# Kernel optimization log

Measured on AMD Instinct MI355X. Metric: run time of the kernel, lower is better.

Reference implementation:

```python
import jax, jax.numpy as jnp
from jax import lax
import numpy as np

EPS_LN = 1e-5
EPS_BN = 1e-5
NEG_SLOPE = 0.01  # MONAI UnetResBlock leaky relu slope


def conv3d(x, w, b=None, padding=0, dilation=1, groups=1):
    # x: [B,C,D1,D2,D3], w: [O, I/groups, k,k,k]
    pads = [(padding, padding)] * 3
    y = lax.conv_general_dilated(x, w, (1, 1, 1), pads,
                                 rhs_dilation=(dilation,) * 3,
                                 dimension_numbers=('NCDHW', 'OIDHW', 'NCDHW'),
                                 feature_group_count=groups)
    if b is not None:
        y = y + b[None, :, None, None, None]
    return y


def _trilinear(x_flat, z, y, xw, D, H, W):
    # x_flat: [B,C,S]; z,y,xw: [B,S] float sample coords. Zero padding outside.
    z0 = jnp.floor(z); y0 = jnp.floor(y); x0 = jnp.floor(xw)
    tz = z - z0; ty = y - y0; tx = xw - x0
    iz0 = z0.astype(jnp.int32); iy0 = y0.astype(jnp.int32); ix0 = x0.astype(jnp.int32)
    gather = jax.vmap(lambda xf, i: jnp.take(xf, i, axis=1))  # over batch
    out = jnp.zeros_like(x_flat)
    for dz in (0, 1):
        for dy in (0, 1):
            for dx in (0, 1):
                zi = iz0 + dz; yi = iy0 + dy; xi = ix0 + dx
                wgt = ((tz if dz else 1.0 - tz) * (ty if dy else 1.0 - ty)
                       * (tx if dx else 1.0 - tx))
                valid = ((zi >= 0) & (zi < D) & (yi >= 0) & (yi < H)
                         & (xi >= 0) & (xi < W))
                idx = (jnp.clip(zi, 0, D - 1) * H + jnp.clip(yi, 0, H - 1)) * W \
                      + jnp.clip(xi, 0, W - 1)
                g = gather(x_flat, idx)  # [B,C,S]
                out = out + g * (wgt * valid)[:, None, :]
    return out


def deform_conv3d(x, off_w, off_b, w, b):
    # DCNv1-style 3D deformable conv, kernel 3x3x3, stride 1, pad 1.
    B, C, D, H, W = x.shape
    S = D * H * W
    off = conv3d(x, off_w, off_b, padding=1)          # [B, 3*27, D,H,W]
    off = off.reshape(B, 27, 3, S)                    # per-tap (dz,dy,dx)
    gz, gy, gx = jnp.meshgrid(jnp.arange(D), jnp.arange(H), jnp.arange(W), indexing='ij')
    gz = gz.reshape(-1).astype(x.dtype)
    gy = gy.reshape(-1).astype(x.dtype)
    gx = gx.reshape(-1).astype(x.dtype)
    x_flat = x.reshape(B, C, S)
    out = jnp.zeros((B, w.shape[0], S), x.dtype)
    k = 0
    for kd in (-1, 0, 1):
        for kh in (-1, 0, 1):
            for kw in (-1, 0, 1):
                z = gz[None, :] + kd + off[:, k, 0]
                y = gy[None, :] + kh + off[:, k, 1]
                xc = gx[None, :] + kw + off[:, k, 2]
                val = _trilinear(x_flat, z, y, xc, D, H, W)  # [B,C,S]
                out = out + jnp.einsum('oc,bcs->bos', w[:, :, kd + 1, kh + 1, kw + 1], val)
                k += 1
    out = out + b[None, :, None]
    return out.reshape(B, w.shape[0], D, H, W)


def _leaky(v):
    return jnp.where(v >= 0, v, NEG_SLOPE * v)


def _bn(v, s, b_, m, var):
    inv = lax.rsqrt(var + EPS_BN)
    return (v - m[None, :, None, None, None]) * (s * inv)[None, :, None, None, None] \
        + b_[None, :, None, None, None]


def reference(x, ln_s, ln_b, gamma,
              p1_w, p1_b, p2_w, p2_b,
              c0_w, c0_b, cs_w, cs_b,
              off_w, off_b, dc_w, dc_b,
              c1_w, c1_b,
              u1_w, bn1_s, bn1_b, bn1_m, bn1_v,
              u2_w, bn2_s, bn2_b, bn2_m, bn2_v,
              pr_w, pr_b):
    B, C, H, W, D = x.shape
    tok = x.reshape(B, C, -1).transpose(0, 2, 1)  # [B, N, C]
    # LayerNorm over C
    mu = jnp.mean(tok, axis=-1, keepdims=True)
    var = jnp.mean((tok - mu) ** 2, axis=-1, keepdims=True)
    xn = (tok - mu) * lax.rsqrt(var + EPS_LN) * ln_s + ln_b
    # _Attention3d_deform
    v = xn.transpose(0, 2, 1).reshape(B, C, H, W, D)
    shortcut = v
    v = conv3d(v, p1_w, p1_b)                 # proj_1 (1x1x1)
    v = jax.nn.gelu(v, approximate=False)
    # _3d_deform spatial gating unit
    u = v
    a = conv3d(v, c0_w, c0_b, padding=2, groups=C)              # 5x5x5 depthwise
    a = conv3d(a, cs_w, cs_b, padding=9, dilation=3, groups=C)  # 7x7x7 dil=3 depthwise
    a = deform_conv3d(a, off_w, off_b, dc_w, dc_b)
    a = conv3d(a, c1_w, c1_b)                 # 1x1x1
    v = u * a
    v = conv3d(v, p2_w, p2_b) + shortcut      # proj_2 + residual
    epa = v.reshape(B, C, -1).transpose(0, 2, 1)
    feat = tok + gamma * epa                  # [B, N, C]
    skip = feat.reshape(B, H, W, D, C).transpose(0, 4, 1, 2, 3)  # [B,C,H,W,D]
    # UnetResBlock (conv-bn-lrelu-conv-bn + residual, lrelu), eval-mode BN
    h = conv3d(skip, u1_w, padding=1)
    h = _leaky(_bn(h, bn1_s, bn1_b, bn1_m, bn1_v))
    h = conv3d(h, u2_w, padding=1)
    h = _bn(h, bn2_s, bn2_b, bn2_m, bn2_v)
    attn = _leaky(h + skip)
    # projconv: Dropout3d is identity in eval; 1x1x1 conv
    out = skip + conv3d(attn, pr_w, pr_b)
    return out


def setup_inputs() -> dict:
    key = jax.random.key(0)
    ks = jax.random.split(key, 16)
    C, Bv, S = 48, 2, 32

    def w(k, shape, s=0.05):
        return jax.random.normal(k, shape, jnp.float32) * s

    return {
        'x': jax.random.normal(ks[0], (Bv, C, S, S, S), jnp.float32),
        'ln_s': jnp.ones((C,), jnp.float32), 'ln_b': jnp.zeros((C,), jnp.float32),
        'gamma': jnp.full((C,), 0.1, jnp.float32),
        'p1_w': w(ks[1], (C, C, 1, 1, 1)), 'p1_b': jnp.zeros((C,), jnp.float32),
        'p2_w': w(ks[2], (C, C, 1, 1, 1)), 'p2_b': jnp.zeros((C,), jnp.float32),
        'c0_w': w(ks[3], (C, 1, 5, 5, 5)), 'c0_b': jnp.zeros((C,), jnp.float32),
        'cs_w': w(ks[4], (C, 1, 7, 7, 7)), 'cs_b': jnp.zeros((C,), jnp.float32),
        'off_w': w(ks[5], (81, C, 3, 3, 3), 0.01), 'off_b': jnp.zeros((81,), jnp.float32),
        'dc_w': w(ks[6], (C, C, 3, 3, 3)), 'dc_b': jnp.zeros((C,), jnp.float32),
        'c1_w': w(ks[7], (C, C, 1, 1, 1)), 'c1_b': jnp.zeros((C,), jnp.float32),
        'u1_w': w(ks[8], (C, C, 3, 3, 3)),
        'bn1_s': jnp.ones((C,), jnp.float32), 'bn1_b': jnp.zeros((C,), jnp.float32),
        'bn1_m': jnp.zeros((C,), jnp.float32), 'bn1_v': jnp.ones((C,), jnp.float32),
        'u2_w': w(ks[9], (C, C, 3, 3, 3)),
        'bn2_s': jnp.ones((C,), jnp.float32), 'bn2_b': jnp.zeros((C,), jnp.float32),
        'bn2_m': jnp.zeros((C,), jnp.float32), 'bn2_v': jnp.ones((C,), jnp.float32),
        'pr_w': w(ks[10], (C, C, 1, 1, 1)), 'pr_b': jnp.zeros((C,), jnp.float32),
    }
```

## Files before the change

kernel.cpp:

```cpp
#include <hip/hip_runtime.h>
#include <hip/hip_fp16.h>
#include <math.h>

#define CCH 48
#define SDIM 32
#define SVOL (SDIM*SDIM*SDIM)
#define NB 2

typedef _Float16 half2_t __attribute__((ext_vector_type(2)));
typedef _Float16 half4_t __attribute__((ext_vector_type(4)));
typedef float float4_t __attribute__((ext_vector_type(4)));

static __device__ __forceinline__ float dot2f(half2_t a, half2_t b, float c) {
#if __has_builtin(__builtin_amdgcn_fdot2)
    return __builtin_amdgcn_fdot2(a, b, c, false);
#else
    return c + (float)a[0] * (float)b[0] + (float)a[1] * (float)b[1];
#endif
}


__global__ __launch_bounds__(256)
void reshape_pair_kernel(const float* __restrict__ w, half2_t* __restrict__ wt, int NO) {
    int i = blockIdx.x * 256 + threadIdx.x;
    int total = 27 * 24 * NO;
    if (i < total) {
        int o = i % NO; int rem = i / NO; int cp = rem % 24; int k = rem / 24;
        float w0 = w[((size_t)o * CCH + 2 * cp) * 27 + k];
        float w1 = w[((size_t)o * CCH + 2 * cp + 1) * 27 + k];
        wt[i] = half2_t{ (_Float16)w0, (_Float16)w1 };
    }
}

__global__ __launch_bounds__(256)
void reshape_mfma_off_kernel(const float* __restrict__ w, half4_t* __restrict__ wA) {
    int e = blockIdx.x * 256 + threadIdx.x;
    if (e < 31104) {
        int row = e & 15;
        int kq = (e >> 4) & 3;
        int ks = (e / 64) % 3;
        int mt = (e / 192) % 6;
        int tap = e / 1152;
        int o = mt * 16 + row;
        half4_t v;
        #pragma unroll
        for (int h = 0; h < 4; h++) {
            int ci = ks * 16 + kq * 4 + h;
            float val = (o < 81) ? w[((size_t)o * CCH + ci) * 27 + tap] : 0.f;
            v[h] = (_Float16)val;
        }
        wA[e] = v;
    }
}

__global__ __launch_bounds__(256)
void reshape_mfma48_kernel(const float* __restrict__ w, half4_t* __restrict__ wA) {
    int e = blockIdx.x * 256 + threadIdx.x;
    if (e < 15552) {
        int row = e & 15;
        int kq = (e >> 4) & 3;
        int ks = (e / 64) % 3;
        int mt = (e / 192) % 3;
        int tap = e / 576;
        int o = mt * 16 + row;
        half4_t v;
        #pragma unroll
        for (int h = 0; h < 4; h++) {
            int ci = ks * 16 + kq * 4 + h;
            v[h] = (_Float16)w[((size_t)o * CCH + ci) * 27 + tap];
        }
        wA[e] = v;
    }
}

__global__ __launch_bounds__(256)
void t1x1_pair_kernel(const float* __restrict__ w, half2_t* __restrict__ wt) {
    int i = blockIdx.x * 256 + threadIdx.x;
    if (i < 24 * CCH) {
        int o = i % CCH, cp = i / CCH;
        wt[i] = half2_t{ (_Float16)w[o * CCH + 2 * cp], (_Float16)w[o * CCH + 2 * cp + 1] };
    }
}

__global__ __launch_bounds__(256)
void t1x1_kernel(const float* __restrict__ w, float* __restrict__ wt) {
    int i = blockIdx.x * 256 + threadIdx.x;
    if (i < CCH * CCH) { int ci = i / CCH, o = i % CCH; wt[i] = w[o * CCH + ci]; }
}

__global__ __launch_bounds__(64)
void cb_kernel(const float* __restrict__ c1w, const float* __restrict__ c1b,
               const float* __restrict__ dcb, float* __restrict__ cb) {
    int o = threadIdx.x;
    if (o < CCH) {
        float v = c1b[o];
        for (int ci = 0; ci < CCH; ci++) v += c1w[o * CCH + ci] * dcb[ci];
        cb[o] = v;
    }
}

__global__ __launch_bounds__(256)
void ln_kernel(const float* __restrict__ x, const float* __restrict__ ln_s,
               const float* __restrict__ ln_b, float* __restrict__ xn,
               half2_t* __restrict__ xnp) {
    int s = blockIdx.x * 256 + threadIdx.x;
    int b = blockIdx.y;
    const float* xb = x + (size_t)b * CCH * SVOL + s;
    float v[CCH];
    float mu = 0.f;
    #pragma unroll
    for (int c = 0; c < CCH; c++) { v[c] = xb[c * SVOL]; mu += v[c]; }
    mu *= (1.0f / CCH);
    float var = 0.f;
    #pragma unroll
    for (int c = 0; c < CCH; c++) { float d = v[c] - mu; var += d * d; }
    var *= (1.0f / CCH);
    float inv = rsqrtf(var + 1e-5f);
    float* o = xn + (size_t)b * CCH * SVOL + s;
    float nv[CCH];
    #pragma unroll
    for (int c = 0; c < CCH; c++) { nv[c] = (v[c] - mu) * inv * ln_s[c] + ln_b[c]; o[c * SVOL] = nv[c]; }
    half2_t* xp = xnp + (size_t)b * 24 * SVOL + s;
    #pragma unroll
    for (int cp = 0; cp < 24; cp++)
        xp[(size_t)cp * SVOL] = half2_t{ (_Float16)nv[2 * cp], (_Float16)nv[2 * cp + 1] };
}

__global__ __launch_bounds__(256, 4)
void p1_gelu_kernel(const half2_t* __restrict__ xnp, const half2_t* __restrict__ wt,
                    const float* __restrict__ bias, float* __restrict__ u) {
    int tid = threadIdx.x;
    int g = blockIdx.y, b = blockIdx.z;
    int s = blockIdx.x * 256 + tid;
    const half2_t* xb = xnp + (size_t)b * 24 * SVOL + s;
    float acc[12];
    #pragma unroll
    for (int o = 0; o < 12; o++) acc[o] = bias[g * 12 + o];
    for (int cp = 0; cp < 24; cp++) {
        half2_t v2 = xb[(size_t)cp * SVOL];
        const half2_t* wr = wt + cp * CCH + g * 12;
        #pragma unroll
        for (int o = 0; o < 12; o++) acc[o] = dot2f(v2, wr[o], acc[o]);
    }
    float* ub = u + (size_t)b * CCH * SVOL + s + (size_t)(g * 12) * SVOL;
    #pragma unroll
    for (int o = 0; o < 12; o++) {
        float a = acc[o];
        ub[o * SVOL] = 0.5f * a * (1.0f + erff(a * 0.70710678118654752f));
    }
}

__global__ __launch_bounds__(256, 4)
void dw5_kernel(const float* __restrict__ in, const float* __restrict__ w,
                const float* __restrict__ bias, float* __restrict__ out) {
    int tid = threadIdx.x;
    int c = blockIdx.y, b = blockIdx.z;
    const float* wc = w + c * 125;
    int bx = blockIdx.x;
    int yx = (bx >> 1) * 256 + tid;
    int z0 = (bx & 1) * 16;
    int y = yx >> 5, xx = yx & 31;
    const float* ib = in + ((size_t)b * CCH + c) * SVOL;
    float acc[16];
    float bv = bias[c];
    #pragma unroll
    for (int z = 0; z < 16; z++) acc[z] = bv;
    for (int ty = 0; ty < 5; ty++) {
        int yy = y + ty - 2; if (yy < 0 || yy >= 32) continue;
        for (int tx = 0; tx < 5; tx++) {
            int xv = xx + tx - 2; if (xv < 0 || xv >= 32) continue;
            const float* col = ib + yy * 32 + xv;
            float cv[20];
            #pragma unroll
            for (int j = 0; j < 20; j++) {
                int zz = z0 - 2 + j;
                cv[j] = (zz >= 0 && zz < 32) ? col[(size_t)zz * 1024] : 0.f;
            }
            #pragma unroll
            for (int tz = 0; tz < 5; tz++) {
                float wv = wc[(tz * 5 + ty) * 5 + tx];
                #pragma unroll
                for (int z = 0; z < 16; z++) acc[z] += wv * cv[z + tz];
            }
        }
    }
    float* ob = out + ((size_t)b * CCH + c) * SVOL + y * 32 + xx;
    #pragma unroll
    for (int z = 0; z < 16; z++) ob[(size_t)(z0 + z) * 1024] = acc[z];
}

__global__ __launch_bounds__(256, 4)
void dw7_kernel(const float* __restrict__ in, const float* __restrict__ w,
                const float* __restrict__ bias, float* __restrict__ out) {
    int tid = threadIdx.x;
    int c = blockIdx.y, b = blockIdx.z;
    const float* wc = w + c * 343;
    int bx = blockIdx.x;
    int yx = (bx >> 1) * 256 + tid;
    int z0 = (bx & 1) * 16;
    int y = yx >> 5, xx = yx & 31;
    const float* ib = in + ((size_t)b * CCH + c) * SVOL;
    float acc[16];
    float bv = bias[c];
    #pragma unroll
    for (int z = 0; z < 16; z++) acc[z] = bv;
    for (int ty = 0; ty < 7; ty++) {
        int yy = y + 3 * (ty - 3); if (yy < 0 || yy >= 32) continue;
        for (int tx = 0; tx < 7; tx++) {
            int xv = xx + 3 * (tx - 3); if (xv < 0 || xv >= 32) continue;
            const float* col = ib + yy * 32 + xv;
            float cv[34];
            #pragma unroll
            for (int j = 0; j < 34; j++) {
                int zz = z0 - 9 + j;
                cv[j] = (zz >= 0 && zz < 32) ? col[(size_t)zz * 1024] : 0.f;
            }
            #pragma unroll
            for (int tz = 0; tz < 7; tz++) {
                float wv = wc[(tz * 7 + ty) * 7 + tx];
                #pragma unroll
                for (int z = 0; z < 16; z++) acc[z] += wv * cv[z + 3 * tz];
            }
        }
    }
    float* ob = out + ((size_t)b * CCH + c) * SVOL + y * 32 + xx;
    #pragma unroll
    for (int z = 0; z < 16; z++) ob[(size_t)(z0 + z) * 1024] = acc[z];
}

__global__ __launch_bounds__(256)
void transpose_pack_kernel(const float* __restrict__ a1, __half* __restrict__ a1h) {
    __shared__ float tile[CCH * 65];
    int tid = threadIdx.x;
    int b = blockIdx.y;
    int s0 = blockIdx.x * 64;
    const float* ib = a1 + (size_t)b * CCH * SVOL + s0;
    for (int i = tid; i < CCH * 64; i += 256) {
        int c = i >> 6, p = i & 63;
        tile[c * 65 + p] = ib[(size_t)c * SVOL + p];
    }
    __syncthreads();
    __half* ob = a1h + ((size_t)b * SVOL + s0) * CCH;
    for (int i = tid; i < 64 * CCH; i += 256) {
        int p = i / CCH, c = i % CCH;
        ob[i] = __float2half(tile[c * 65 + p]);
    }
}

__global__ __launch_bounds__(256, 4)
void offconv_mfma_kernel(const __half* __restrict__ a1h, const half4_t* __restrict__ wA,
                         float* __restrict__ off) {
    __shared__ __half halo[216 * 52];
    int tid = threadIdx.x;
    int t = blockIdx.x;
    int b = blockIdx.y;
    int tz0 = (t >> 6) * 4, ty0 = ((t >> 3) & 7) * 4, tx0 = (t & 7) * 4;
    const __half* ab = a1h + (size_t)b * SVOL * CCH;
    for (int idx = tid; idx < 216 * 24; idx += 256) {
        int hpos = idx / 24, kp = idx % 24;
        int hz = hpos / 36, hy = (hpos / 6) % 6, hx = hpos % 6;
        int gz = tz0 + hz - 1, gy = ty0 + hy - 1, gx = tx0 + hx - 1;
        unsigned int v = 0u;
        if (gz >= 0 && gz < 32 && gy >= 0 && gy < 32 && gx >= 0 && gx < 32) {
            int s = (gz * 32 + gy) * 32 + gx;
            v = *reinterpret_cast<const unsigned int*>(ab + (size_t)s * CCH + kp * 2);
        }
        *reinterpret_cast<unsigned int*>(&halo[hpos * 52 + kp * 2]) = v;
    }
    __syncthreads();
    int wave = tid >> 6, lane = tid & 63;
    int col = lane & 15;
    int kq = lane >> 4;
    int py = col >> 2, px = col & 3;
    int pz = wave;
    float4_t acc[6];
    #pragma unroll
    for (int m = 0; m < 6; m++) acc[m] = (float4_t)0.f;
    for (int tap = 0; tap < 27; tap++) {
        int dz = tap / 9, dy = (tap / 3) % 3, dx = tap % 3;
        int hbase = ((pz + dz) * 36 + (py + dy) * 6 + (px + dx)) * 52 + kq * 4;
        half4_t bf0 = *reinterpret_cast<const half4_t*>(&halo[hbase]);
        half4_t bf1 = *reinterpret_cast<const half4_t*>(&halo[hbase + 16]);
        half4_t bf2 = *reinterpret_cast<const half4_t*>(&halo[hbase + 32]);
        #pragma unroll
        for (int mt = 0; mt < 6; mt++) {
            int fb = (tap * 6 + mt) * 12 + kq;
            half4_t a0 = wA[(size_t)fb * 16 + col];
            half4_t a1 = wA[(size_t)(fb + 4) * 16 + col];
            half4_t a2 = wA[(size_t)(fb + 8) * 16 + col];
            acc[mt] = __builtin_amdgcn_mfma_f32_16x16x16f16(a0, bf0, acc[mt], 0, 0, 0);
            acc[mt] = __builtin_amdgcn_mfma_f32_16x16x16f16(a1, bf1, acc[mt], 0, 0, 0);
            acc[mt] = __builtin_amdgcn_mfma_f32_16x16x16f16(a2, bf2, acc[mt], 0, 0, 0);
        }
    }
    int sg = ((tz0 + pz) * 32 + ty0 + py) * 32 + tx0 + px;
    float* ob = off + (size_t)b * 81 * SVOL + sg;
    #pragma unroll
    for (int mt = 0; mt < 6; mt++) {
        #pragma unroll
        for (int r = 0; r < 4; r++) {
            int orow = mt * 16 + kq * 4 + r;
            if (orow < 81) ob[(size_t)orow * SVOL] = acc[mt][r];
        }
    }
}

__global__ __launch_bounds__(256, 4)
void u1_mfma_kernel(const __half* __restrict__ skh, const half4_t* __restrict__ wA,
                    const float* __restrict__ bs, const float* __restrict__ bb,
                    const float* __restrict__ bm, const float* __restrict__ bv,
                    __half* __restrict__ h1h) {
    __shared__ __half halo[216 * 52];
    int tid = threadIdx.x;
    int t = blockIdx.x;
    int b = blockIdx.y;
    int tz0 = (t >> 6) * 4, ty0 = ((t >> 3) & 7) * 4, tx0 = (t & 7) * 4;
    const __half* ab = skh + (size_t)b * SVOL * CCH;
    for (int idx = tid; idx < 216 * 24; idx += 256) {
        int hpos = idx / 24, kp = idx % 24;
        int hz = hpos / 36, hy = (hpos / 6) % 6, hx = hpos % 6;
        int gz = tz0 + hz - 1, gy = ty0 + hy - 1, gx = tx0 + hx - 1;
        unsigned int v = 0u;
        if (gz >= 0 && gz < 32 && gy >= 0 && gy < 32 && gx >= 0 && gx < 32) {
            int s = (gz * 32 + gy) * 32 + gx;
            v = *reinterpret_cast<const unsigned int*>(ab + (size_t)s * CCH + kp * 2);
        }
        *reinterpret_cast<unsigned int*>(&halo[hpos * 52 + kp * 2]) = v;
    }
    __syncthreads();
    int wave = tid >> 6, lane = tid & 63;
    int col = lane & 15;
    int kq = lane >> 4;
    int py = col >> 2, px = col & 3;
    int pz = wave;
    float4_t acc[3];
    #pragma unroll
    for (int m = 0; m < 3; m++) acc[m] = (float4_t)0.f;
    for (int tap = 0; tap < 27; tap++) {
        int dz = tap / 9, dy = (tap / 3) % 3, dx = tap % 3;
        int hbase = ((pz + dz) * 36 + (py + dy) * 6 + (px + dx)) * 52 + kq * 4;
        half4_t bf0 = *reinterpret_cast<const half4_t*>(&halo[hbase]);
        half4_t bf1 = *reinterpret_cast<const half4_t*>(&halo[hbase + 16]);
        half4_t bf2 = *reinterpret_cast<const half4_t*>(&halo[hbase + 32]);
        #pragma unroll
        for (int mt = 0; mt < 3; mt++) {
            int fb = (tap * 3 + mt) * 12 + kq;
            half4_t a0 = wA[(size_t)fb * 16 + col];
            half4_t a1 = wA[(size_t)(fb + 4) * 16 + col];
            half4_t a2 = wA[(size_t)(fb + 8) * 16 + col];
            acc[mt] = __builtin_amdgcn_mfma_f32_16x16x16f16(a0, bf0, acc[mt], 0, 0, 0);
            acc[mt] = __builtin_amdgcn_mfma_f32_16x16x16f16(a1, bf1, acc[mt], 0, 0, 0);
            acc[mt] = __builtin_amdgcn_mfma_f32_16x16x16f16(a2, bf2, acc[mt], 0, 0, 0);
        }
    }
    int sg = ((tz0 + pz) * 32 + ty0 + py) * 32 + tx0 + px;
    __half* ob = h1h + ((size_t)b * SVOL + sg) * CCH;
    #pragma unroll
    for (int mt = 0; mt < 3; mt++) {
        float hv[4];
        #pragma unroll
        for (int r = 0; r < 4; r++) {
            int orow = mt * 16 + kq * 4 + r;
            float inv = rsqrtf(bv[orow] + 1e-5f);
            float h = (acc[mt][r] - bm[orow]) * (bs[orow] * inv) + bb[orow];
            hv[r] = h >= 0.f ? h : 0.01f * h;
        }
        half2_t* po = reinterpret_cast<half2_t*>(ob + mt * 16 + kq * 4);
        po[0] = half2_t{ (_Float16)hv[0], (_Float16)hv[1] };
        po[1] = half2_t{ (_Float16)hv[2], (_Float16)hv[3] };
    }
}

__global__ __launch_bounds__(256, 4)
void u2_mfma_kernel(const __half* __restrict__ h1h, const float* __restrict__ skip,
                    const half4_t* __restrict__ wA,
                    const float* __restrict__ bs, const float* __restrict__ bb,
                    const float* __restrict__ bm, const float* __restrict__ bv,
                    __half* __restrict__ attnh) {
    __shared__ __half halo[216 * 52];
    int tid = threadIdx.x;
    int t = blockIdx.x;
    int b = blockIdx.y;
    int tz0 = (t >> 6) * 4, ty0 = ((t >> 3) & 7) * 4, tx0 = (t & 7) * 4;
    const __half* ab = h1h + (size_t)b * SVOL * CCH;
    for (int idx = tid; idx < 216 * 24; idx += 256) {
        int hpos = idx / 24, kp = idx % 24;
        int hz = hpos / 36, hy = (hpos / 6) % 6, hx = hpos % 6;
        int gz = tz0 + hz - 1, gy = ty0 + hy - 1, gx = tx0 + hx - 1;
        unsigned int v = 0u;
        if (gz >= 0 && gz < 32 && gy >= 0 && gy < 32 && gx >= 0 && gx < 32) {
            int s = (gz * 32 + gy) * 32 + gx;
            v = *reinterpret_cast<const unsigned int*>(ab + (size_t)s * CCH + kp * 2);
        }
        *reinterpret_cast<unsigned int*>(&halo[hpos * 52 + kp * 2]) = v;
    }
    __syncthreads();
    int wave = tid >> 6, lane = tid & 63;
    int col = lane & 15;
    int kq = lane >> 4;
    int py = col >> 2, px = col & 3;
    int pz = wave;
    float4_t acc[3];
    #pragma unroll
    for (int m = 0; m < 3; m++) acc[m] = (float4_t)0.f;
    for (int tap = 0; tap < 27; tap++) {
        int dz = tap / 9, dy = (tap / 3) % 3, dx = tap % 3;
        int hbase = ((pz + dz) * 36 + (py + dy) * 6 + (px + dx)) * 52 + kq * 4;
        half4_t bf0 = *reinterpret_cast<const half4_t*>(&halo[hbase]);
        half4_t bf1 = *reinterpret_cast<const half4_t*>(&halo[hbase + 16]);
        half4_t bf2 = *reinterpret_cast<const half4_t*>(&halo[hbase + 32]);
        #pragma unroll
        for (int mt = 0; mt < 3; mt++) {
            int fb = (tap * 3 + mt) * 12 + kq;
            half4_t a0 = wA[(size_t)fb * 16 + col];
            half4_t a1 = wA[(size_t)(fb + 4) * 16 + col];
            half4_t a2 = wA[(size_t)(fb + 8) * 16 + col];
            acc[mt] = __builtin_amdgcn_mfma_f32_16x16x16f16(a0, bf0, acc[mt], 0, 0, 0);
            acc[mt] = __builtin_amdgcn_mfma_f32_16x16x16f16(a1, bf1, acc[mt], 0, 0, 0);
            acc[mt] = __builtin_amdgcn_mfma_f32_16x16x16f16(a2, bf2, acc[mt], 0, 0, 0);
        }
    }
    int sg = ((tz0 + pz) * 32 + ty0 + py) * 32 + tx0 + px;
    const float* sk = skip + (size_t)b * CCH * SVOL + sg;
    __half* ob = attnh + ((size_t)b * SVOL + sg) * CCH;
    #pragma unroll
    for (int mt = 0; mt < 3; mt++) {
        float av[4];
        #pragma unroll
        for (int r = 0; r < 4; r++) {
            int orow = mt * 16 + kq * 4 + r;
            float inv = rsqrtf(bv[orow] + 1e-5f);
            float h = (acc[mt][r] - bm[orow]) * (bs[orow] * inv) + bb[orow];
            float a = h + sk[(size_t)orow * SVOL];
            av[r] = a >= 0.f ? a : 0.01f * a;
        }
        half2_t* po = reinterpret_cast<half2_t*>(ob + mt * 16 + kq * 4);
        po[0] = half2_t{ (_Float16)av[0], (_Float16)av[1] };
        po[1] = half2_t{ (_Float16)av[2], (_Float16)av[3] };
    }
}

struct h8v { half2_t a, b, c, d; };

__global__ __launch_bounds__(256, 4)
void deform_kernel(const __half* __restrict__ a1h, const float* __restrict__ off,
                   const float* __restrict__ off_b,
                   const half2_t* __restrict__ wt, float* __restrict__ out) {
    int tid = threadIdx.x;
    int gc = blockIdx.y;
    int b = blockIdx.z;
    int s = blockIdx.x * 256 + tid;
    int z = s >> 10, y = (s >> 5) & 31, xx = s & 31;
    const __half* abase = a1h + (size_t)b * SVOL * CCH + gc * 16;
    const float* ob = off + (size_t)b * 81 * SVOL + s;
    float acc[CCH];
    #pragma unroll
    for (int o = 0; o < CCH; o++) acc[o] = 0.f;
    for (int k = 0; k < 27; k++) {
        int kd = k / 9 - 1, kh = (k / 3) % 3 - 1, kw = k % 3 - 1;
        float zf = (float)(z + kd) + ob[(size_t)(k * 3 + 0) * SVOL] + off_b[k * 3 + 0];
        float yf = (float)(y + kh) + ob[(size_t)(k * 3 + 1) * SVOL] + off_b[k * 3 + 1];
        float xf = (float)(xx + kw) + ob[(size_t)(k * 3 + 2) * SVOL] + off_b[k * 3 + 2];
        float z0 = floorf(zf), y0 = floorf(yf), x0 = floorf(xf);
        float tz = zf - z0, ty = yf - y0, tx = xf - x0;
        int iz0 = (int)z0, iy0 = (int)y0, ix0 = (int)x0;
        half2_t val2[8];
        #pragma unroll
        for (int j = 0; j < 8; j++) val2[j] = (half2_t)(_Float16)0;
        #pragma unroll
        for (int corner = 0; corner < 8; corner++) {
            int dz = corner >> 2, dy = (corner >> 1) & 1, dx = corner & 1;
            int zi = iz0 + dz, yi = iy0 + dy, xi = ix0 + dx;
            bool valid = (zi >= 0 && zi < 32 && yi >= 0 && yi < 32 && xi >= 0 && xi < 32);
            float wgt = (dz ? tz : 1.f - tz) * (dy ? ty : 1.f - ty) * (dx ? tx : 1.f - tx);
            float cwv = valid ? wgt : 0.f;
            _Float16 cwh = (_Float16)cwv;
            half2_t cw2 = { cwh, cwh };
            int zc = min(max(zi, 0), 31), yc = min(max(yi, 0), 31), xc = min(max(xi, 0), 31);
            int cidx = (zc * 32 + yc) * 32 + xc;
            const h8v* pv = (const h8v*)(abase + (size_t)cidx * CCH);
            h8v q0 = pv[0], q1 = pv[1];
            val2[0] += cw2 * q0.a;  val2[1] += cw2 * q0.b;
            val2[2] += cw2 * q0.c;  val2[3] += cw2 * q0.d;
            val2[4] += cw2 * q1.a;  val2[5] += cw2 * q1.b;
            val2[6] += cw2 * q1.c;  val2[7] += cw2 * q1.d;
        }
        #pragma unroll
        for (int cpl = 0; cpl < 8; cpl++) {
            half2_t v2 = val2[cpl];
            const half2_t* wr = wt + ((size_t)k * 24 + gc * 8 + cpl) * CCH;
            #pragma unroll
            for (int o = 0; o < CCH; o++) acc[o] = dot2f(v2, wr[o], acc[o]);
        }
    }
    float* op = out + (size_t)b * CCH * SVOL + s;
    #pragma unroll
    for (int o = 0; o < CCH; o++) atomicAdd(&op[(size_t)o * SVOL], acc[o]);
}

__global__ __launch_bounds__(256, 4)
void gate1_kernel(const float* __restrict__ dc, const float* __restrict__ u,
                  const float* __restrict__ wt, const float* __restrict__ cb,
                  half2_t* __restrict__ a2p) {
    int tid = threadIdx.x;
    int g = blockIdx.y, b = blockIdx.z;
    int s = blockIdx.x * 256 + tid;
    size_t base = (size_t)b * CCH * SVOL + s;
    float acc[12];
    #pragma unroll
    for (int o = 0; o < 12; o++) acc[o] = cb[g * 12 + o];
    for (int ci = 0; ci < CCH; ci++) {
        float v = dc[base + (size_t)ci * SVOL];
        const float* wr = wt + ci * CCH + g * 12;
        #pragma unroll
        for (int o = 0; o < 12; o++) acc[o] += wr[o] * v;
    }
    #pragma unroll
    for (int o = 0; o < 12; o++) acc[o] *= u[base + (size_t)(g * 12 + o) * SVOL];
    half2_t* ap = a2p + ((size_t)b * 24 + g * 6) * SVOL + s;
    #pragma unroll
    for (int j = 0; j < 6; j++)
        ap[(size_t)j * SVOL] = half2_t{ (_Float16)acc[2 * j], (_Float16)acc[2 * j + 1] };
}

__global__ __launch_bounds__(256, 4)
void gate2_kernel(const half2_t* __restrict__ a2p, const float* __restrict__ xn,
                  const float* __restrict__ x,
                  const half2_t* __restrict__ wt, const float* __restrict__ p2b,
                  const float* __restrict__ gamma, float* __restrict__ skip,
                  __half* __restrict__ skh) {
    int tid = threadIdx.x;
    int g = blockIdx.y, b = blockIdx.z;
    int s = blockIdx.x * 256 + tid;
    size_t base = (size_t)b * CCH * SVOL + s;
    const half2_t* ab = a2p + (size_t)b * 24 * SVOL + s;
    float acc[12];
    #pragma unroll
    for (int o = 0; o < 12; o++) acc[o] = p2b[g * 12 + o];
    for (int cp = 0; cp < 24; cp++) {
        half2_t v2 = ab[(size_t)cp * SVOL];
        const half2_t* wr = wt + cp * CCH + g * 12;
        #pragma unroll
        for (int o = 0; o < 12; o++) acc[o] = dot2f(v2, wr[o], acc[o]);
    }
    float sv[12];
    #pragma unroll
    for (int o = 0; o < 12; o++) {
        int oc = g * 12 + o;
        float vv = acc[o] + xn[base + (size_t)oc * SVOL];
        sv[o] = x[base + (size_t)oc * SVOL] + gamma[oc] * vv;
        skip[base + (size_t)oc * SVOL] = sv[o];
    }
    half2_t* sh = reinterpret_cast<half2_t*>(skh + ((size_t)b * SVOL + s) * CCH + g * 12);
    #pragma unroll
    for (int j = 0; j < 6; j++)
        sh[j] = half2_t{ (_Float16)sv[2 * j], (_Float16)sv[2 * j + 1] };
}

__global__ __launch_bounds__(256, 4)
void pr_final_kernel(const __half* __restrict__ attnh, const float* __restrict__ skip,
                     const half2_t* __restrict__ wt, const float* __restrict__ prb,
                     float* __restrict__ out) {
    int tid = threadIdx.x;
    int g = blockIdx.y, b = blockIdx.z;
    int s = blockIdx.x * 256 + tid;
    size_t base = (size_t)b * CCH * SVOL + s;
    const half2_t* ab = reinterpret_cast<const half2_t*>(attnh + ((size_t)b * SVOL + s) * CCH);
    float acc[12];
    #pragma unroll
    for (int o = 0; o < 12; o++) acc[o] = prb[g * 12 + o];
    for (int cp = 0; cp < 24; cp++) {
        half2_t v2 = ab[cp];
        const half2_t* wr = wt + cp * CCH + g * 12;
        #pragma unroll
        for (int o = 0; o < 12; o++) acc[o] = dot2f(v2, wr[o], acc[o]);
    }
    #pragma unroll
    for (int o = 0; o < 12; o++) {
        int oc = g * 12 + o;
        out[base + (size_t)oc * SVOL] = skip[base + (size_t)oc * SVOL] + acc[o];
    }
}

extern "C" void kernel_launch(void* const* d_in, const int* in_sizes, int n_in,
                              void* d_out, int out_size, void* d_ws, size_t ws_size,
                              hipStream_t stream) {
    (void)in_sizes; (void)n_in; (void)out_size; (void)ws_size;
    const float* x     = (const float*)d_in[0];
    const float* ln_s  = (const float*)d_in[1];
    const float* ln_b  = (const float*)d_in[2];
    const float* gamma = (const float*)d_in[3];
    const float* p1_w  = (const float*)d_in[4];
    const float* p1_b  = (const float*)d_in[5];
    const float* p2_w  = (const float*)d_in[6];
    const float* p2_b  = (const float*)d_in[7];
    const float* c0_w  = (const float*)d_in[8];
    const float* c0_b  = (const float*)d_in[9];
    const float* cs_w  = (const float*)d_in[10];
    const float* cs_b  = (const float*)d_in[11];
    const float* off_w = (const float*)d_in[12];
    const float* off_b = (const float*)d_in[13];
    const float* dc_w  = (const float*)d_in[14];
    const float* dc_b  = (const float*)d_in[15];
    const float* c1_w  = (const float*)d_in[16];
    const float* c1_b  = (const float*)d_in[17];
    const float* u1_w  = (const float*)d_in[18];
    const float* bn1_s = (const float*)d_in[19];
    const float* bn1_b = (const float*)d_in[20];
    const float* bn1_m = (const float*)d_in[21];
    const float* bn1_v = (const float*)d_in[22];
    const float* u2_w  = (const float*)d_in[23];
    const float* bn2_s = (const float*)d_in[24];
    const float* bn2_b = (const float*)d_in[25];
    const float* bn2_m = (const float*)d_in[26];
    const float* bn2_v = (const float*)d_in[27];
    const float* pr_w  = (const float*)d_in[28];
    const float* pr_b  = (const float*)d_in[29];
    float* out = (float*)d_out;

    float* wsf = (float*)d_ws;
    const size_t TS = (size_t)NB * CCH * SVOL;
    float* xn   = out;
    float* ubuf = wsf;
    float* bufA = wsf + TS;
    float* bufB = wsf + 2 * TS;
    float* offb = wsf + 3 * TS;
    float* wtb    = wsf + 3 * TS + (size_t)NB * 81 * SVOL;
    float* wt_offf = wtb;
    float* wt_dcf  = wt_offf + 104976;
    float* wt_u1f  = wt_dcf + 62208;
    float* wt_u2f  = wt_u1f + 62208;
    float* pt_p1  = wt_u2f + 62208;
    float* pt_c1  = pt_p1 + 2304;
    float* pt_p2  = pt_c1 + 2304;
    float* pt_pr  = pt_p2 + 2304;
    float* cb_all = pt_pr + 2304;

    __half*  a1h = (__half*)bufA;
    __half*  skh = (__half*)ubuf;
    __half*  h1h = (__half*)(ubuf + TS / 2);
    half2_t* xnp = (half2_t*)bufB;
    half2_t* a2p = (half2_t*)offb;
    __half*  attnh = (__half*)offb;
    half4_t* wA_off = (half4_t*)wt_offf;
    half2_t* wt_dch  = (half2_t*)wt_dcf;
    half4_t* wA_u1 = (half4_t*)wt_u1f;
    half4_t* wA_u2 = (half4_t*)wt_u2f;
    half2_t* wt_p1h  = (half2_t*)pt_p1;
    half2_t* wt_p2h  = (half2_t*)pt_p2;
    half2_t* wt_prh  = (half2_t*)pt_pr;

    dim3 blk(256);
    dim3 gpos(SVOL / 256, NB);
    dim3 g4(SVOL / 256, 4, NB);
    dim3 gmf(512, NB);
    dim3 g3d(SVOL / 256, 3, NB);
    dim3 gdwc(8, CCH, NB);
    dim3 gtr(SVOL / 64, NB);

    hipLaunchKernelGGL(reshape_mfma_off_kernel, dim3((31104 + 255) / 256), blk, 0, stream, off_w, wA_off);
    hipLaunchKernelGGL(reshape_mfma48_kernel, dim3((15552 + 255) / 256), blk, 0, stream, u1_w, wA_u1);
    hipLaunchKernelGGL(reshape_mfma48_kernel, dim3((15552 + 255) / 256), blk, 0, stream, u2_w, wA_u2);
    hipLaunchKernelGGL(reshape_pair_kernel, dim3((27 * 24 * 48 + 255) / 256), blk, 0, stream, dc_w, wt_dch, 48);
    hipLaunchKernelGGL(t1x1_pair_kernel, dim3(5), blk, 0, stream, p1_w, wt_p1h);
    hipLaunchKernelGGL(t1x1_pair_kernel, dim3(5), blk, 0, stream, p2_w, wt_p2h);
    hipLaunchKernelGGL(t1x1_pair_kernel, dim3(5), blk, 0, stream, pr_w, wt_prh);
    hipLaunchKernelGGL(t1x1_kernel, dim3(9), blk, 0, stream, c1_w, pt_c1);
    hipLaunchKernelGGL(cb_kernel, dim3(1), dim3(64), 0, stream, c1_w, c1_b, dc_b, cb_all);

    hipLaunchKernelGGL(ln_kernel,            gpos, blk, 0, stream, x, ln_s, ln_b, xn, xnp);
    hipLaunchKernelGGL(p1_gelu_kernel,       g4,   blk, 0, stream, xnp, wt_p1h, p1_b, ubuf);
    hipLaunchKernelGGL(dw5_kernel,           gdwc, blk, 0, stream, ubuf, c0_w, c0_b, bufA);
    hipLaunchKernelGGL(dw7_kernel,           gdwc, blk, 0, stream, bufA, cs_w, cs_b, bufB);
    hipLaunchKernelGGL(transpose_pack_kernel, gtr, blk, 0, stream, bufB, a1h);
    hipLaunchKernelGGL(offconv_mfma_kernel,  gmf,  blk, 0, stream, a1h, wA_off, offb);
    hipMemsetAsync(bufB, 0, TS * sizeof(float), stream);
    hipLaunchKernelGGL(deform_kernel,        g3d,  blk, 0, stream, a1h, offb, off_b, wt_dch, bufB);
    hipLaunchKernelGGL(gate1_kernel,         g4,   blk, 0, stream, bufB, ubuf, pt_c1, cb_all, a2p);
    hipLaunchKernelGGL(gate2_kernel,         g4,   blk, 0, stream, a2p, xn, x, wt_p2h, p2_b, gamma,
                       bufA, skh);
    hipLaunchKernelGGL(u1_mfma_kernel,       gmf,  blk, 0, stream, skh, wA_u1,
                       bn1_s, bn1_b, bn1_m, bn1_v, h1h);
    hipLaunchKernelGGL(u2_mfma_kernel,       gmf,  blk, 0, stream, h1h, bufA, wA_u2,
                       bn2_s, bn2_b, bn2_m, bn2_v, attnh);
    hipLaunchKernelGGL(pr_final_kernel,      g4,   blk, 0, stream, attnh, bufA, wt_prh, pr_b, out);
}
```

Before: 504.5 us.

## Use MFMA for deformable conv channel contraction via LDS-staged samples

The per-thread fdot2 accumulation over 48 output channels in the deformable conv is replaced by 16x16x16 f16 MFMA tiles. Each thread still computes its trilinear-sampled 16-channel vector, writes it to a double-buffered shared tile, and the wave reads it back as the B operand against pre-reshaped weight fragments. This cuts the scalar FMA work and the register pressure of 48 accumulators, at the cost of LDS traffic and a new weight layout. There is no explicit barrier, which relies on each wave reading only its own LDS region.

```diff
diff --git a/kernel.cpp b/kernel.cpp
--- a/kernel.cpp
+++ b/kernel.cpp
@@ -19,18 +19,6 @@
 #endif
 }
 
-
-__global__ __launch_bounds__(256)
-void reshape_pair_kernel(const float* __restrict__ w, half2_t* __restrict__ wt, int NO) {
-    int i = blockIdx.x * 256 + threadIdx.x;
-    int total = 27 * 24 * NO;
-    if (i < total) {
-        int o = i % NO; int rem = i / NO; int cp = rem % 24; int k = rem / 24;
-        float w0 = w[((size_t)o * CCH + 2 * cp) * 27 + k];
-        float w1 = w[((size_t)o * CCH + 2 * cp + 1) * 27 + k];
-        wt[i] = half2_t{ (_Float16)w0, (_Float16)w1 };
-    }
-}
 
 __global__ __launch_bounds__(256)
 void reshape_mfma_off_kernel(const float* __restrict__ w, half4_t* __restrict__ wA) {
@@ -67,6 +55,26 @@
         #pragma unroll
         for (int h = 0; h < 4; h++) {
             int ci = ks * 16 + kq * 4 + h;
+            v[h] = (_Float16)w[((size_t)o * CCH + ci) * 27 + tap];
+        }
+        wA[e] = v;
+    }
+}
+
+__global__ __launch_bounds__(256)
+void reshape_mfma_dc_kernel(const float* __restrict__ w, half4_t* __restrict__ wA) {
+    int e = blockIdx.x * 256 + threadIdx.x;
+    if (e < 15552) {
+        int row = e & 15;
+        int kq = (e >> 4) & 3;
+        int mt = (e / 64) % 3;
+        int tap = (e / 192) % 27;
+        int gc = e / 5184;
+        int o = mt * 16 + row;
+        half4_t v;
+        #pragma unroll
+        for (int h = 0; h < 4; h++) {
+            int ci = gc * 16 + kq * 4 + h;
             v[h] = (_Float16)w[((size_t)o * CCH + ci) * 27 + tap];
         }
         wA[e] = v;
@@ -443,19 +451,24 @@
 struct h8v { half2_t a, b, c, d; };
 
 __global__ __launch_bounds__(256, 4)
-void deform_kernel(const __half* __restrict__ a1h, const float* __restrict__ off,
-                   const float* __restrict__ off_b,
-                   const half2_t* __restrict__ wt, float* __restrict__ out) {
+void deform_mfma_kernel(const __half* __restrict__ a1h, const float* __restrict__ off,
+                        const float* __restrict__ off_b,
+                        const half4_t* __restrict__ wA, float* __restrict__ out) {
+    __shared__ __half vbuf[2][4][64][20];
     int tid = threadIdx.x;
     int gc = blockIdx.y;
     int b = blockIdx.z;
+    int wave = tid >> 6, lane = tid & 63;
+    int col = lane & 15, kq = lane >> 4;
     int s = blockIdx.x * 256 + tid;
     int z = s >> 10, y = (s >> 5) & 31, xx = s & 31;
     const __half* abase = a1h + (size_t)b * SVOL * CCH + gc * 16;
     const float* ob = off + (size_t)b * 81 * SVOL + s;
-    float acc[CCH];
-    #pragma unroll
-    for (int o = 0; o < CCH; o++) acc[o] = 0.f;
+    float4_t acc[3][4];
+    #pragma unroll
+    for (int m = 0; m < 3; m++)
+        #pragma unroll
+        for (int c = 0; c < 4; c++) acc[m][c] = (float4_t)0.f;
     for (int k = 0; k < 27; k++) {
         int kd = k / 9 - 1, kh = (k / 3) % 3 - 1, kw = k % 3 - 1;
         float zf = (float)(z + kd) + ob[(size_t)(k * 3 + 0) * SVOL] + off_b[k * 3 + 0];
@@ -485,17 +498,41 @@
             val2[4] += cw2 * q1.a;  val2[5] += cw2 * q1.b;
             val2[6] += cw2 * q1.c;  val2[7] += cw2 * q1.d;
         }
-        #pragma unroll
-        for (int cpl = 0; cpl < 8; cpl++) {
-            half2_t v2 = val2[cpl];
-            const half2_t* wr = wt + ((size_t)k * 24 + gc * 8 + cpl) * CCH;
+        __half* vb = &vbuf[k & 1][wave][lane][0];
+        half4_t* vb4 = reinterpret_cast<half4_t*>(vb);
+        vb4[0] = half4_t{ val2[0][0], val2[0][1], val2[1][0], val2[1][1] };
+        vb4[1] = half4_t{ val2[2][0], val2[2][1], val2[3][0], val2[3][1] };
+        vb4[2] = half4_t{ val2[4][0], val2[4][1], val2[5][0], val2[5][1] };
+        vb4[3] = half4_t{ val2[6][0], val2[6][1], val2[7][0], val2[7][1] };
+        half4_t a0, a1, a2;
+        {
+            int fb = ((gc * 27 + k) * 3 + 0) * 4 + kq;
+            a0 = wA[(size_t)fb * 16 + col];
+            a1 = wA[(size_t)(fb + 4) * 16 + col];
+            a2 = wA[(size_t)(fb + 8) * 16 + col];
+        }
+        #pragma unroll
+        for (int ct = 0; ct < 4; ct++) {
+            half4_t bf = *reinterpret_cast<const half4_t*>(&vbuf[k & 1][wave][ct * 16 + col][kq * 4]);
+            acc[0][ct] = __builtin_amdgcn_mfma_f32_16x16x16f16(a0, bf, acc[0][ct], 0, 0, 0);
+            acc[1][ct] = __builtin_amdgcn_mfma_f32_16x16x16f16(a1, bf, acc[1][ct], 0, 0, 0);
+            acc[2][ct] = __builtin_amdgcn_mfma_f32_16x16x16f16(a2, bf, acc[2][ct], 0, 0, 0);
+        }
+    }
+    int sbase = blockIdx.x * 256 + wave * 64;
+    float* op = out + (size_t)b * CCH * SVOL;
+    #pragma unroll
+    for (int mt = 0; mt < 3; mt++) {
+        #pragma unroll
+        for (int ct = 0; ct < 4; ct++) {
+            int sp = sbase + ct * 16 + col;
             #pragma unroll
-            for (int o = 0; o < CCH; o++) acc[o] = dot2f(v2, wr[o], acc[o]);
-        }
-    }
-    float* op = out + (size_t)b * CCH * SVOL + s;
-    #pragma unroll
-    for (int o = 0; o < CCH; o++) atomicAdd(&op[(size_t)o * SVOL], acc[o]);
+            for (int r = 0; r < 4; r++) {
+                int o = mt * 16 + kq * 4 + r;
+                atomicAdd(&op[(size_t)o * SVOL + sp], acc[mt][ct][r]);
+            }
+        }
+    }
 }
 
 __global__ __launch_bounds__(256, 4)
@@ -643,7 +680,7 @@
     half2_t* a2p = (half2_t*)offb;
     __half*  attnh = (__half*)offb;
     half4_t* wA_off = (half4_t*)wt_offf;
-    half2_t* wt_dch  = (half2_t*)wt_dcf;
+    half4_t* wA_dc  = (half4_t*)wt_dcf;
     half4_t* wA_u1 = (half4_t*)wt_u1f;
     half4_t* wA_u2 = (half4_t*)wt_u2f;
     half2_t* wt_p1h  = (half2_t*)pt_p1;
@@ -661,7 +698,7 @@
     hipLaunchKernelGGL(reshape_mfma_off_kernel, dim3((31104 + 255) / 256), blk, 0, stream, off_w, wA_off);
     hipLaunchKernelGGL(reshape_mfma48_kernel, dim3((15552 + 255) / 256), blk, 0, stream, u1_w, wA_u1);
     hipLaunchKernelGGL(reshape_mfma48_kernel, dim3((15552 + 255) / 256), blk, 0, stream, u2_w, wA_u2);
-    hipLaunchKernelGGL(reshape_pair_kernel, dim3((27 * 24 * 48 + 255) / 256), blk, 0, stream, dc_w, wt_dch, 48);
+    hipLaunchKernelGGL(reshape_mfma_dc_kernel, dim3((15552 + 255) / 256), blk, 0, stream, dc_w, wA_dc);
     hipLaunchKernelGGL(t1x1_pair_kernel, dim3(5), blk, 0, stream, p1_w, wt_p1h);
     hipLaunchKernelGGL(t1x1_pair_kernel, dim3(5), blk, 0, stream, p2_w, wt_p2h);
     hipLaunchKernelGGL(t1x1_pair_kernel, dim3(5), blk, 0, stream, pr_w, wt_prh);
@@ -675,7 +712,7 @@
     hipLaunchKernelGGL(transpose_pack_kernel, gtr, blk, 0, stream, bufB, a1h);
     hipLaunchKernelGGL(offconv_mfma_kernel,  gmf,  blk, 0, stream, a1h, wA_off, offb);
     hipMemsetAsync(bufB, 0, TS * sizeof(float), stream);
-    hipLaunchKernelGGL(deform_kernel,        g3d,  blk, 0, stream, a1h, offb, off_b, wt_dch, bufB);
+    hipLaunchKernelGGL(deform_mfma_kernel,   g3d,  blk, 0, stream, a1h, offb, off_b, wA_dc, bufB);
     hipLaunchKernelGGL(gate1_kernel,         g4,   blk, 0, stream, bufB, ubuf, pt_c1, cb_all, a2p);
     hipLaunchKernelGGL(gate2_kernel,         g4,   blk, 0, stream, a2p, xn, x, wt_p2h, p2_b, gamma,
                        bufA, skh);
```

After: 483.3 us. 1.04x faster.
